# Optimization experiments

Measured on AMD Instinct MI355X. Metric: run time of the kernel, lower is better.

## Reference

```python
import jax, jax.numpy as jnp
import numpy as np

B, C, L = 8, 256, 2048


def setup_inputs() -> dict:
    key = jax.random.key(0)
    ks = jax.random.split(key, 7)
    s = 0.05
    return {
        "x": jax.random.normal(ks[0], (B, C, L), dtype=jnp.float32),
        "Wq": jax.random.normal(ks[1], (C, C), dtype=jnp.float32) * s,
        "bq": jax.random.normal(ks[2], (C,), dtype=jnp.float32) * s,
        "Wk": jax.random.normal(ks[3], (C, C), dtype=jnp.float32) * s,
        "bk": jax.random.normal(ks[4], (C,), dtype=jnp.float32) * s,
        "Wv": jax.random.normal(ks[5], (C, C), dtype=jnp.float32) * s,
        "bv": jax.random.normal(ks[6], (C,), dtype=jnp.float32) * s,
    }


def reference(x, Wq, bq, Wk, bk, Wv, bv):
    # Conv1d with kernel_size=1 == per-position linear over channels.
    # x: [B, C, L]
    scale = x.shape[1] ** (-0.5)
    q = jnp.einsum('oc,bcl->bol', Wq, x) + bq[None, :, None]  # [B,C,L]
    k = jnp.einsum('oc,bcl->bol', Wk, x) + bk[None, :, None]
    v = jnp.einsum('oc,bcl->bol', Wv, x) + bv[None, :, None]
    scores = jnp.einsum('bcl,bcm->blm', q, k) * scale          # [B,L,L]
    attn = jax.nn.softmax(scores, axis=-1)
    context = jnp.einsum('blm,bcm->bcl', attn, v)              # [B,C,L]
    return context + x
```

## Files before the change

kernel.cpp:

```cpp
#include <hip/hip_runtime.h>

#define NB 8
#define NC 256
#define NL 2048
#define SCALE 0.0625f

typedef __attribute__((ext_vector_type(8))) __bf16 bf16x8;
typedef __attribute__((ext_vector_type(4))) float f32x4;
typedef __attribute__((ext_vector_type(4))) unsigned int u32x4;
typedef __attribute__((ext_vector_type(4))) unsigned short u16x4;
typedef __attribute__((ext_vector_type(8))) unsigned short u16x8;

static __device__ __forceinline__ unsigned short f2b(float f) {
    unsigned int u = __builtin_bit_cast(unsigned int, f);
    u += 0x7fffu + ((u >> 16) & 1u);
    return (unsigned short)(u >> 16);
}

__global__ void wconv_kernel(const float* __restrict__ Wq,
                             const float* __restrict__ Wk,
                             const float* __restrict__ Wv,
                             unsigned short* __restrict__ Wbf)
{
    const int base = (blockIdx.x * 256 + threadIdx.x) * 4;
    const int mat  = base >> 16;
    const int off  = base & 65535;
    const float* W = (mat == 0) ? Wq : (mat == 1) ? Wk : Wv;
    float4 w = *(const float4*)&W[off];
    u16x4 p = {f2b(w.x), f2b(w.y), f2b(w.z), f2b(w.w)};
    *(u16x4*)&Wbf[base] = p;
}

__global__ __launch_bounds__(256, 2) void xprep_kernel(
    const float* __restrict__ x, unsigned short* __restrict__ xT)
{
    const int b  = blockIdx.z;
    const int c0 = blockIdx.y * 64;
    const int l0 = blockIdx.x * 64;
    const int t  = threadIdx.x;

    __shared__ unsigned short Tr[64][68];

    #pragma unroll
    for (int p = 0; p < 4; ++p) {
        const int c  = p * 16 + (t >> 4);
        const int lg = t & 15;
        float4 xv = *(const float4*)&x[((size_t)(b * NC + c0 + c)) * NL + l0 + lg * 4];
        u16x4 pk = {f2b(xv.x), f2b(xv.y), f2b(xv.z), f2b(xv.w)};
        *(u16x4*)&Tr[c][lg * 4] = pk;
    }
    __syncthreads();
    #pragma unroll
    for (int j = 0; j < 2; ++j) {
        const int chunk = t + 256 * j;
        const int l  = chunk >> 3;
        const int ck = chunk & 7;
        u16x8 o;
        #pragma unroll
        for (int i = 0; i < 8; ++i) o[i] = Tr[ck * 8 + i][l];
        *(u16x8*)&xT[((size_t)(b * NL + l0 + l)) * NC + c0 + ck * 8] = o;
    }
}

__global__ __launch_bounds__(256, 2) void qkv_mfma(
    const unsigned short* __restrict__ xT,
    const unsigned short* __restrict__ Wbf,
    const float* __restrict__ bq, const float* __restrict__ bk,
    const float* __restrict__ bv,
    unsigned short* __restrict__ qT, unsigned short* __restrict__ kT,
    unsigned short* __restrict__ vo)
{
    const int raw = blockIdx.x;
    const int b   = raw & 7;
    const int rem = raw >> 3;
    const int mat = rem >> 5;
    const int lt0 = (rem & 31) * 64;
    const int t    = threadIdx.x;
    const int w    = t >> 6;
    const int lane = t & 63;
    const int ln15 = lane & 15;
    const int quad = lane >> 4;

    __shared__ __align__(16) unsigned short XT[64 * 256];
    __shared__ __align__(16) unsigned short WC[256 * 64];

    const unsigned short* Wm = Wbf + mat * 65536;
    const float* bias = (mat == 0) ? bq : (mat == 1) ? bk : bv;

    float bvals[4][4];
    #pragma unroll
    for (int ot = 0; ot < 4; ++ot)
        #pragma unroll
        for (int r = 0; r < 4; ++r)
            bvals[ot][r] = bias[w * 64 + ot * 16 + quad * 4 + r];

    #pragma unroll
    for (int s = 0; s < 8; ++s) {
        const int il = w * 8 + s;
        const int n  = il * 2 + (lane >> 5);
        const int p  = lane & 31;
        const int g  = p ^ (n & 15);
        const unsigned short* gp = &xT[((size_t)(b * NL + lt0 + n)) * NC + g * 8];
        __builtin_amdgcn_global_load_lds(
            (const __attribute__((address_space(1))) unsigned int*)gp,
            (__attribute__((address_space(3))) unsigned int*)&XT[il * 512],
            16, 0, 0);
    }

    f32x4 acc[4][4];
    #pragma unroll
    for (int i = 0; i < 4; ++i)
        #pragma unroll
        for (int j = 0; j < 4; ++j) acc[i][j] = f32x4{0.f, 0.f, 0.f, 0.f};

    for (int k0 = 0; k0 < 4; ++k0) {
        if (k0) __syncthreads();
        #pragma unroll
        for (int s = 0; s < 8; ++s) {
            const int il = w * 8 + s;
            const int o  = il * 8 + (lane >> 3);
            const int p  = lane & 7;
            const int g  = p ^ (o & 7);
            const unsigned short* gp = &Wm[(size_t)o * NC + k0 * 64 + g * 8];
            __builtin_amdgcn_global_load_lds(
                (const __attribute__((address_space(1))) unsigned int*)gp,
                (__attribute__((address_space(3))) unsigned int*)&WC[il * 512],
                16, 0, 0);
        }
        __syncthreads();

        #pragma unroll
        for (int ks = 0; ks < 2; ++ks) {
            bf16x8 xf[4];
            #pragma unroll
            for (int lt = 0; lt < 4; ++lt) {
                const int l  = lt * 16 + ln15;
                const int kc = k0 * 8 + ks * 4 + quad;
                const int pp = kc ^ (l & 15);
                xf[lt] = __builtin_bit_cast(bf16x8, *(const u32x4*)&XT[l * 256 + pp * 8]);
            }
            #pragma unroll
            for (int ot = 0; ot < 4; ++ot) {
                const int o  = w * 64 + ot * 16 + ln15;
                const int pp = (ks * 4 + quad) ^ (o & 7);
                bf16x8 wf = __builtin_bit_cast(bf16x8, *(const u32x4*)&WC[o * 64 + pp * 8]);
                #pragma unroll
                for (int lt = 0; lt < 4; ++lt)
                    acc[ot][lt] = __builtin_amdgcn_mfma_f32_16x16x32_bf16(
                                      wf, xf[lt], acc[ot][lt], 0, 0, 0);
            }
        }
    }

    if (mat < 2) {
        unsigned short* out = (mat == 0) ? qT : kT;
        #pragma unroll
        for (int ot = 0; ot < 4; ++ot) {
            const int o_base = w * 64 + ot * 16 + quad * 4;
            #pragma unroll
            for (int lt = 0; lt < 4; ++lt) {
                const int l = lt0 + lt * 16 + ln15;
                u16x4 pk;
                #pragma unroll
                for (int r = 0; r < 4; ++r)
                    pk[r] = f2b(acc[ot][lt][r] + bvals[ot][r]);
                *(u16x4*)&out[((size_t)(b * NL + l)) * NC + o_base] = pk;
            }
        }
    } else {
        #pragma unroll
        for (int ot = 0; ot < 4; ++ot)
            #pragma unroll
            for (int lt = 0; lt < 4; ++lt) {
                const int l = lt0 + lt * 16 + ln15;
                #pragma unroll
                for (int r = 0; r < 4; ++r) {
                    const int o = w * 64 + ot * 16 + quad * 4 + r;
                    vo[((size_t)(b * NC + o)) * NL + l] = f2b(acc[ot][lt][r] + bvals[ot][r]);
                }
            }
    }
}

__global__ __launch_bounds__(512, 1) void attn_kernel(
    const unsigned short* __restrict__ qT,
    const unsigned short* __restrict__ kT,
    const unsigned short* __restrict__ v,
    const float* __restrict__ x,
    float* __restrict__ out)
{
    const int raw  = blockIdx.x;
    const int b    = raw & 7;
    const int l0   = (raw >> 3) * 64;
    const int t    = threadIdx.x;
    const int w    = t >> 6;
    const int lane = t & 63;
    const int ln15 = lane & 15;
    const int quad = lane >> 4;
    const int qg   = w & 3;
    const int kg   = w >> 2;

    __shared__ __align__(16) char smem[139776];
    unsigned short* Kb0 = (unsigned short*)smem;
    unsigned short* Kb1 = (unsigned short*)(smem + 32768);
    unsigned short* Vb0 = (unsigned short*)(smem + 65536);
    unsigned short* Vb1 = (unsigned short*)(smem + 98304);
    unsigned short* Plds = (unsigned short*)(smem + 131072);
    float* denomP = (float*)(smem + 139264);
    float (*ctxbuf)[68] = (float(*)[68])smem;

    bf16x8 qf[8];
    {
        const size_t qrow = ((size_t)b * NL + l0 + qg * 16 + ln15) * NC;
        #pragma unroll
        for (int kt = 0; kt < 8; ++kt)
            qf[kt] = __builtin_bit_cast(bf16x8,
                        *(const u32x4*)&qT[qrow + kt * 32 + quad * 8]);
    }

    f32x4 ctx[16];
    #pragma unroll
    for (int i = 0; i < 16; ++i) ctx[i] = f32x4{0.f, 0.f, 0.f, 0.f};
    float dacc[4] = {0.f, 0.f, 0.f, 0.f};

    auto stage = [&](int mt, unsigned short* Kd, unsigned short* Vd) {
        const int m0 = mt * 64;
        #pragma unroll
        for (int s = 0; s < 4; ++s) {
            const int il = w * 4 + s;
            const int n  = il * 2 + (lane >> 5);
            const int g  = (lane & 31) ^ (n & 15);
            const unsigned short* gp = &kT[((size_t)b * NL + m0 + n) * NC + g * 8];
            __builtin_amdgcn_global_load_lds(
                (const __attribute__((address_space(1))) unsigned int*)gp,
                (__attribute__((address_space(3))) unsigned int*)&Kd[il * 512],
                16, 0, 0);
        }
        #pragma unroll
        for (int s = 0; s < 4; ++s) {
            const int il = w * 4 + s;
            const int c  = il * 8 + (lane >> 3);
            const int g  = (lane & 7) ^ (c & 7);
            const unsigned short* gp = &v[((size_t)(b * NC + c)) * NL + m0 + g * 8];
            __builtin_amdgcn_global_load_lds(
                (const __attribute__((address_space(1))) unsigned int*)gp,
                (__attribute__((address_space(3))) unsigned int*)&Vd[il * 512],
                16, 0, 0);
        }
    };

    stage(0, Kb0, Vb0);
    __syncthreads();

    for (int mt = 0; mt < 32; ++mt) {
        if (mt < 31) {
            if (mt & 1) stage(mt + 1, Kb0, Vb0);
            else        stage(mt + 1, Kb1, Vb1);
        }
        const unsigned short* Kd = (mt & 1) ? Kb1 : Kb0;
        const unsigned short* Vd = (mt & 1) ? Vb1 : Vb0;

        f32x4 sacc[2];
        sacc[0] = f32x4{0.f, 0.f, 0.f, 0.f};
        sacc[1] = f32x4{0.f, 0.f, 0.f, 0.f};
        #pragma unroll
        for (int nt = 0; nt < 2; ++nt) {
            const int n = kg * 32 + nt * 16 + ln15;
            #pragma unroll
            for (int kt = 0; kt < 8; ++kt) {
                const int p = (kt * 4 + quad) ^ ln15;
                bf16x8 bf = __builtin_bit_cast(bf16x8,
                              *(const u32x4*)&Kd[n * 256 + p * 8]);
                sacc[nt] = __builtin_amdgcn_mfma_f32_16x16x32_bf16(
                               qf[kt], bf, sacc[nt], 0, 0, 0);
            }
        }

        float rs[4] = {0.f, 0.f, 0.f, 0.f};
        #pragma unroll
        for (int nt = 0; nt < 2; ++nt) {
            #pragma unroll
            for (int r = 0; r < 4; ++r) {
                float e = __expf(sacc[nt][r] * SCALE);
                rs[r] += e;
                const int ip = qg * 16 + quad * 4 + r;
                const int j  = kg * 32 + nt * 16 + ln15;
                const int pc = (j >> 3) ^ (ip & 7);
                Plds[ip * 64 + pc * 8 + (j & 7)] = f2b(e);
            }
        }
        #pragma unroll
        for (int r = 0; r < 4; ++r) {
            rs[r] += __shfl_xor(rs[r], 1, 64);
            rs[r] += __shfl_xor(rs[r], 2, 64);
            rs[r] += __shfl_xor(rs[r], 4, 64);
            rs[r] += __shfl_xor(rs[r], 8, 64);
            dacc[r] += rs[r];
        }

        bf16x8 pf;
        {
            const int m = qg * 16 + ln15;
            const int p = (kg * 4 + quad) ^ (m & 7);
            pf = __builtin_bit_cast(bf16x8, *(const u32x4*)&Plds[m * 64 + p * 8]);
        }
        #pragma unroll
        for (int ct = 0; ct < 16; ++ct) {
            const int c = ct * 16 + ln15;
            const int p = (kg * 4 + quad) ^ (c & 7);
            bf16x8 vb = __builtin_bit_cast(bf16x8,
                          *(const u32x4*)&Vd[c * 64 + p * 8]);
            ctx[ct] = __builtin_amdgcn_mfma_f32_16x16x32_bf16(
                          pf, vb, ctx[ct], 0, 0, 0);
        }

        __syncthreads();
    }

    if (kg == 1) {
        #pragma unroll
        for (int ct = 0; ct < 16; ++ct) {
            const int c = ct * 16 + ln15;
            #pragma unroll
            for (int r = 0; r < 4; ++r)
                ctxbuf[c][qg * 16 + quad * 4 + r] = ctx[ct][r];
        }
    }
    if (ln15 == 0) {
        #pragma unroll
        for (int r = 0; r < 4; ++r)
            denomP[kg * 64 + qg * 16 + quad * 4 + r] = dacc[r];
    }
    __syncthreads();
    if (kg == 0) {
        float rinv[4];
        #pragma unroll
        for (int r = 0; r < 4; ++r) {
            const int ql = qg * 16 + quad * 4 + r;
            rinv[r] = 1.0f / (denomP[ql] + denomP[64 + ql]);
        }
        #pragma unroll
        for (int ct = 0; ct < 16; ++ct) {
            const int c = ct * 16 + ln15;
            #pragma unroll
            for (int r = 0; r < 4; ++r) {
                const int ql = qg * 16 + quad * 4 + r;
                ctxbuf[c][ql] = (ctx[ct][r] + ctxbuf[c][ql]) * rinv[r];
            }
        }
    }
    __syncthreads();

    #pragma unroll
    for (int p = 0; p < 8; ++p) {
        const int f  = t + 512 * p;
        const int c  = f >> 4;
        const int lg = (f & 15) * 4;
        const size_t idx = ((size_t)(b * NC + c)) * NL + l0 + lg;
        float4 xv = *(const float4*)&x[idx];
        float4 cv = *(const float4*)&ctxbuf[c][lg];
        float4 o = make_float4(cv.x + xv.x, cv.y + xv.y, cv.z + xv.z, cv.w + xv.w);
        *(float4*)&out[idx] = o;
    }
}

extern "C" void kernel_launch(void* const* d_in, const int* in_sizes, int n_in,
                              void* d_out, int out_size, void* d_ws, size_t ws_size,
                              hipStream_t stream) {
    const float* x  = (const float*)d_in[0];
    const float* Wq = (const float*)d_in[1];
    const float* bq = (const float*)d_in[2];
    const float* Wk = (const float*)d_in[3];
    const float* bk = (const float*)d_in[4];
    const float* Wv = (const float*)d_in[5];
    const float* bv = (const float*)d_in[6];
    float* out = (float*)d_out;

    const size_t plane = (size_t)NB * NC * NL;
    unsigned short* qT  = (unsigned short*)d_ws;
    unsigned short* kT  = qT + plane;
    unsigned short* v   = kT + plane;
    unsigned short* xT  = v + plane;
    unsigned short* Wbf = xT + plane;

    wconv_kernel<<<192, 256, 0, stream>>>(Wq, Wk, Wv, Wbf);

    dim3 gx(NL / 64, NC / 64, NB);
    xprep_kernel<<<gx, 256, 0, stream>>>(x, xT);

    qkv_mfma<<<768, 256, 0, stream>>>(xT, Wbf, bq, bk, bv, qT, kT, v);

    attn_kernel<<<256, 512, 0, stream>>>(qT, kT, v, x, out);
}
```

Before: 165.2 us.

## Split attention key tile across four wave groups with 1024-thread blocks

Doubles the attention block to 1024 threads. Each of four key-groups computes a 16-key slice of the score tile, and the PV MFMA is masked by lane so each group contributes only its own keys. Row sums are now computed by an MFMA against a ones vector, replacing the shuffle reductions. The final reduction merges four partial context accumulators through two LDS buffers. This raises wave-level parallelism per CU and halves per-wave staging loads, at the cost of extra reduction syncs and MFMA work wasted on zeroed lanes. The launch-bounds occupancy hint of 4 is unrealistic for 1024 threads and ~137KB of LDS.

New measurement: 236.2 us. +43.0%, slower.

```diff
diff --git a/kernel.cpp b/kernel.cpp
--- a/kernel.cpp
+++ b/kernel.cpp
@@ -182,7 +182,7 @@
     }
 }
 
-__global__ __launch_bounds__(512, 1) void attn_kernel(
+__global__ __launch_bounds__(1024, 4) void attn_kernel(
     const unsigned short* __restrict__ qT,
     const unsigned short* __restrict__ kT,
     const unsigned short* __restrict__ v,
@@ -199,15 +199,17 @@
     const int quad = lane >> 4;
     const int qg   = w & 3;
     const int kg   = w >> 2;
-
-    __shared__ __align__(16) char smem[139776];
+    const int kp   = kg >> 1;
+
+    __shared__ __align__(16) char smem[140288];
     unsigned short* Kb0 = (unsigned short*)smem;
     unsigned short* Kb1 = (unsigned short*)(smem + 32768);
     unsigned short* Vb0 = (unsigned short*)(smem + 65536);
     unsigned short* Vb1 = (unsigned short*)(smem + 98304);
     unsigned short* Plds = (unsigned short*)(smem + 131072);
     float* denomP = (float*)(smem + 139264);
-    float (*ctxbuf)[68] = (float(*)[68])smem;
+    float (*bufA)[68] = (float(*)[68])smem;
+    float (*bufB)[68] = (float(*)[68])(smem + 69632);
 
     bf16x8 qf[8];
     {
@@ -221,13 +223,19 @@
     f32x4 ctx[16];
     #pragma unroll
     for (int i = 0; i < 16; ++i) ctx[i] = f32x4{0.f, 0.f, 0.f, 0.f};
-    float dacc[4] = {0.f, 0.f, 0.f, 0.f};
+    f32x4 dacc = f32x4{0.f, 0.f, 0.f, 0.f};
+
+    const u16x8 ones_u = {0x3F80, 0x3F80, 0x3F80, 0x3F80,
+                          0x3F80, 0x3F80, 0x3F80, 0x3F80};
+    const bf16x8 onesf = __builtin_bit_cast(bf16x8, ones_u);
+
+    const bool live = ((quad >> 1) == (kg & 1));
 
     auto stage = [&](int mt, unsigned short* Kd, unsigned short* Vd) {
         const int m0 = mt * 64;
         #pragma unroll
-        for (int s = 0; s < 4; ++s) {
-            const int il = w * 4 + s;
+        for (int s = 0; s < 2; ++s) {
+            const int il = w * 2 + s;
             const int n  = il * 2 + (lane >> 5);
             const int g  = (lane & 31) ^ (n & 15);
             const unsigned short* gp = &kT[((size_t)b * NL + m0 + n) * NC + g * 8];
@@ -237,8 +245,8 @@
                 16, 0, 0);
         }
         #pragma unroll
-        for (int s = 0; s < 4; ++s) {
-            const int il = w * 4 + s;
+        for (int s = 0; s < 2; ++s) {
+            const int il = w * 2 + s;
             const int c  = il * 8 + (lane >> 3);
             const int g  = (lane & 7) ^ (c & 7);
             const unsigned short* gp = &v[((size_t)(b * NC + c)) * NL + m0 + g * 8];
@@ -260,76 +268,82 @@
         const unsigned short* Kd = (mt & 1) ? Kb1 : Kb0;
         const unsigned short* Vd = (mt & 1) ? Vb1 : Vb0;
 
-        f32x4 sacc[2];
-        sacc[0] = f32x4{0.f, 0.f, 0.f, 0.f};
-        sacc[1] = f32x4{0.f, 0.f, 0.f, 0.f};
-        #pragma unroll
-        for (int nt = 0; nt < 2; ++nt) {
-            const int n = kg * 32 + nt * 16 + ln15;
-            #pragma unroll
-            for (int kt = 0; kt < 8; ++kt) {
-                const int p = (kt * 4 + quad) ^ ln15;
-                bf16x8 bf = __builtin_bit_cast(bf16x8,
-                              *(const u32x4*)&Kd[n * 256 + p * 8]);
-                sacc[nt] = __builtin_amdgcn_mfma_f32_16x16x32_bf16(
-                               qf[kt], bf, sacc[nt], 0, 0, 0);
-            }
-        }
-
-        float rs[4] = {0.f, 0.f, 0.f, 0.f};
-        #pragma unroll
-        for (int nt = 0; nt < 2; ++nt) {
-            #pragma unroll
-            for (int r = 0; r < 4; ++r) {
-                float e = __expf(sacc[nt][r] * SCALE);
-                rs[r] += e;
-                const int ip = qg * 16 + quad * 4 + r;
-                const int j  = kg * 32 + nt * 16 + ln15;
-                const int pc = (j >> 3) ^ (ip & 7);
-                Plds[ip * 64 + pc * 8 + (j & 7)] = f2b(e);
-            }
-        }
+        f32x4 sacc = f32x4{0.f, 0.f, 0.f, 0.f};
+        const int n = kg * 16 + ln15;
+        #pragma unroll
+        for (int kt = 0; kt < 8; ++kt) {
+            const int p = (kt * 4 + quad) ^ ln15;
+            bf16x8 bf = __builtin_bit_cast(bf16x8,
+                          *(const u32x4*)&Kd[n * 256 + p * 8]);
+            sacc = __builtin_amdgcn_mfma_f32_16x16x32_bf16(
+                       qf[kt], bf, sacc, 0, 0, 0);
+        }
+
         #pragma unroll
         for (int r = 0; r < 4; ++r) {
-            rs[r] += __shfl_xor(rs[r], 1, 64);
-            rs[r] += __shfl_xor(rs[r], 2, 64);
-            rs[r] += __shfl_xor(rs[r], 4, 64);
-            rs[r] += __shfl_xor(rs[r], 8, 64);
-            dacc[r] += rs[r];
+            float e = __expf(sacc[r] * SCALE);
+            const int ip = qg * 16 + quad * 4 + r;
+            const int j  = kg * 16 + ln15;
+            const int pc = (j >> 3) ^ (ip & 7);
+            Plds[ip * 64 + pc * 8 + (j & 7)] = f2b(e);
         }
 
         bf16x8 pf;
         {
-            const int m = qg * 16 + ln15;
-            const int p = (kg * 4 + quad) ^ (m & 7);
-            pf = __builtin_bit_cast(bf16x8, *(const u32x4*)&Plds[m * 64 + p * 8]);
-        }
+            const int m  = qg * 16 + ln15;
+            const int jc = kg * 2 + (quad & 1);
+            u32x4 pw = *(const u32x4*)&Plds[m * 64 + (jc ^ (m & 7)) * 8];
+            u32x4 pz = live ? pw : u32x4{0u, 0u, 0u, 0u};
+            pf = __builtin_bit_cast(bf16x8, pz);
+        }
+
+        dacc = __builtin_amdgcn_mfma_f32_16x16x32_bf16(pf, onesf, dacc, 0, 0, 0);
+
+        #pragma unroll
+        for (int ct = 0; ct < 16; ++ct) {
+            const int c  = ct * 16 + ln15;
+            const int pv = (kp * 4 + quad) ^ (c & 7);
+            bf16x8 vb = __builtin_bit_cast(bf16x8,
+                          *(const u32x4*)&Vd[c * 64 + pv * 8]);
+            ctx[ct] = __builtin_amdgcn_mfma_f32_16x16x32_bf16(
+                          pf, vb, ctx[ct], 0, 0, 0);
+        }
+
+        __syncthreads();
+    }
+
+    if (ln15 == 0) {
+        #pragma unroll
+        for (int r = 0; r < 4; ++r)
+            denomP[kg * 64 + qg * 16 + quad * 4 + r] = dacc[r];
+    }
+    if (kg == 3) {
         #pragma unroll
         for (int ct = 0; ct < 16; ++ct) {
             const int c = ct * 16 + ln15;
-            const int p = (kg * 4 + quad) ^ (c & 7);
-            bf16x8 vb = __builtin_bit_cast(bf16x8,
-                          *(const u32x4*)&Vd[c * 64 + p * 8]);
-            ctx[ct] = __builtin_amdgcn_mfma_f32_16x16x32_bf16(
-                          pf, vb, ctx[ct], 0, 0, 0);
-        }
-
-        __syncthreads();
-    }
-
-    if (kg == 1) {
+            #pragma unroll
+            for (int r = 0; r < 4; ++r)
+                bufA[c][qg * 16 + quad * 4 + r] = ctx[ct][r];
+        }
+    }
+    if (kg == 2) {
         #pragma unroll
         for (int ct = 0; ct < 16; ++ct) {
             const int c = ct * 16 + ln15;
             #pragma unroll
             for (int r = 0; r < 4; ++r)
-                ctxbuf[c][qg * 16 + quad * 4 + r] = ctx[ct][r];
-        }
-    }
-    if (ln15 == 0) {
-        #pragma unroll
-        for (int r = 0; r < 4; ++r)
-            denomP[kg * 64 + qg * 16 + quad * 4 + r] = dacc[r];
+                bufB[c][qg * 16 + quad * 4 + r] = ctx[ct][r];
+        }
+    }
+    __syncthreads();
+    if (kg == 1) {
+        #pragma unroll
+        for (int ct = 0; ct < 16; ++ct) {
+            const int c = ct * 16 + ln15;
+            #pragma unroll
+            for (int r = 0; r < 4; ++r)
+                bufA[c][qg * 16 + quad * 4 + r] += ctx[ct][r];
+        }
     }
     __syncthreads();
     if (kg == 0) {
@@ -337,7 +351,8 @@
         #pragma unroll
         for (int r = 0; r < 4; ++r) {
             const int ql = qg * 16 + quad * 4 + r;
-            rinv[r] = 1.0f / (denomP[ql] + denomP[64 + ql]);
+            rinv[r] = 1.0f / (denomP[ql] + denomP[64 + ql] +
+                              denomP[128 + ql] + denomP[192 + ql]);
         }
         #pragma unroll
         for (int ct = 0; ct < 16; ++ct) {
@@ -345,20 +360,20 @@
             #pragma unroll
             for (int r = 0; r < 4; ++r) {
                 const int ql = qg * 16 + quad * 4 + r;
-                ctxbuf[c][ql] = (ctx[ct][r] + ctxbuf[c][ql]) * rinv[r];
+                bufA[c][ql] = (ctx[ct][r] + bufA[c][ql] + bufB[c][ql]) * rinv[r];
             }
         }
     }
     __syncthreads();
 
     #pragma unroll
-    for (int p = 0; p < 8; ++p) {
-        const int f  = t + 512 * p;
+    for (int p = 0; p < 4; ++p) {
+        const int f  = t + 1024 * p;
         const int c  = f >> 4;
         const int lg = (f & 15) * 4;
         const size_t idx = ((size_t)(b * NC + c)) * NL + l0 + lg;
         float4 xv = *(const float4*)&x[idx];
-        float4 cv = *(const float4*)&ctxbuf[c][lg];
+        float4 cv = *(const float4*)&bufA[c][lg];
         float4 o = make_float4(cv.x + xv.x, cv.y + xv.y, cv.z + xv.z, cv.w + xv.w);
         *(float4*)&out[idx] = o;
     }
@@ -390,5 +405,5 @@
 
     qkv_mfma<<<768, 256, 0, stream>>>(xT, Wbf, bq, bk, bv, qT, kT, v);
 
-    attn_kernel<<<256, 512, 0, stream>>>(qT, kT, v, x, out);
-}
+    attn_kernel<<<256, 1024, 0, stream>>>(qT, kT, v, x, out);
+}
```
